# Performance work log

Hardware: AMD Instinct MI355X
Metric: run time of the kernel (lower is better)

## Reference

```python
import jax, jax.numpy as jnp
import numpy as np

B, LQ, LK = 8, 256, 256
Q_SIZE = K_SIZE = H = D_V = 256
MASK_VALUE = -1000000.0


def setup_inputs() -> dict:
    key = jax.random.key(0)
    kq, kk, kv, kl, kwq, kwk, kwv = jax.random.split(key, 7)
    # Linear weights, torch nn.Linear stores (out, in); init ~ U(-1/sqrt(in), 1/sqrt(in))
    def lin(k, out_f, in_f):
        bound = 1.0 / np.sqrt(in_f)
        return jax.random.uniform(k, (out_f, in_f), jnp.float32, -bound, bound)
    return {
        "queries": jax.random.normal(kq, (B, LQ, Q_SIZE), jnp.float32),
        "keyes": jax.random.normal(kk, (B, LK, K_SIZE), jnp.float32),
        "values": jax.random.normal(kv, (B, LK, D_V), jnp.float32),
        "valid_lens": jax.random.randint(kl, (B,), 1, LK + 1),
        "W_q": lin(kwq, H, Q_SIZE),
        "W_k": lin(kwk, H, K_SIZE),
        "W_v": lin(kwv, 1, H),
    }


def reference(queries, keyes, values, valid_lens, W_q, W_k, W_v):
    # Projections (nn.Linear without bias): x @ W.T
    q = jnp.einsum("bqd,hd->bqh", queries, W_q)            # (B, Lq, H)
    k = jnp.einsum("bkd,hd->bkh", keyes, W_k)              # (B, Lk, H)
    # Broadcast-add + tanh: (B, Lq, Lk, H)
    features = jnp.tanh(q[:, :, None, :] + k[:, None, :, :])
    # W_v reduction H -> 1, squeeze: scores (B, Lq, Lk)
    scores = jnp.einsum("bqkh,h->bqk", features, W_v[0])
    # sequence_mask over the last (key) axis with value -1e6
    lk = scores.shape[-1]
    mask = jnp.arange(lk)[None, None, :] < valid_lens[:, None, None]  # (B,1,Lk)
    scores = jnp.where(mask, scores, MASK_VALUE)
    # NOTE: this repo's masked_softmax normalizes over dim=1 (the query axis),
    # faithfully reproduced here.
    attention_weights = jax.nn.softmax(scores, axis=1)
    # dropout is identity in eval / p=0.0
    return jnp.einsum("bqk,bkd->bqd", attention_weights, values)
```

## Files before the change

kernel.cpp:

```cpp
#include <hip/hip_runtime.h>

typedef float vf4 __attribute__((ext_vector_type(4)));

#define LOG2E 1.4426950408889634f
#define TWO_LOG2E 2.8853900817779268f

__device__ __forceinline__ float fexp2(float x) { return __builtin_amdgcn_exp2f(x); }
__device__ __forceinline__ float frcp(float x) { return __builtin_amdgcn_rcpf(x); }

__global__ __launch_bounds__(256) void proj_kernel(
    const float* __restrict__ queries, const float* __restrict__ keyes,
    const float* __restrict__ Wq, const float* __restrict__ Wk,
    float* __restrict__ QpH, float* __restrict__ KpH,
    float* __restrict__ Rsum) {
  __shared__ alignas(16) float At[16 * 68];
  __shared__ alignas(16) float Bt[16 * 68];
  const int t = threadIdx.x;
  if (blockIdx.x == 0 && blockIdx.y == 0 && blockIdx.z == 0) {
    *(vf4*)&Rsum[t * 8] = (vf4){0.f, 0.f, 0.f, 0.f};
    *(vf4*)&Rsum[t * 8 + 4] = (vf4){0.f, 0.f, 0.f, 0.f};
  }
  const int m0 = blockIdx.x * 64;
  const int n0 = blockIdx.y * 64;
  const int k0 = blockIdx.z * 128;
  const bool isQ = (m0 < 2048);
  const float* X = isQ ? queries : keyes;
  const float* W = isQ ? Wq : Wk;
  float* C = (isQ ? QpH : KpH) + blockIdx.z * 524288;
  const int mb = isQ ? m0 : (m0 - 2048);

  const int lm = t >> 2;
  const int lq = t & 3;
  const int mm4 = (t & 15) * 4;
  const int nn4 = (t >> 4) * 4;

  float acc[4][4] = {};
  for (int kc = k0; kc < k0 + 128; kc += 16) {
    __syncthreads();
    vf4 xa = *(const vf4*)&X[(mb + lm) * 256 + kc + lq * 4];
    vf4 wb = *(const vf4*)&W[(n0 + lm) * 256 + kc + lq * 4];
#pragma unroll
    for (int c = 0; c < 4; ++c) {
      At[(lq * 4 + c) * 68 + lm] = xa[c];
      Bt[(lq * 4 + c) * 68 + lm] = wb[c];
    }
    __syncthreads();
#pragma unroll
    for (int kk = 0; kk < 16; ++kk) {
      vf4 a4 = *(const vf4*)&At[kk * 68 + mm4];
      vf4 b4 = *(const vf4*)&Bt[kk * 68 + nn4];
#pragma unroll
      for (int i = 0; i < 4; ++i)
#pragma unroll
        for (int j = 0; j < 4; ++j) acc[i][j] += a4[i] * b4[j];
    }
  }
#pragma unroll
  for (int i = 0; i < 4; ++i) {
    vf4 o = {fexp2(acc[i][0] * TWO_LOG2E), fexp2(acc[i][1] * TWO_LOG2E),
             fexp2(acc[i][2] * TWO_LOG2E), fexp2(acc[i][3] * TWO_LOG2E)};
    *(vf4*)&C[(mb + mm4 + i) * 256 + n0 + nn4] = o;
  }
}

__global__ __launch_bounds__(256) void scores_exp_kernel(
    const float* __restrict__ QpH, const float* __restrict__ KpH,
    const float* __restrict__ Wv, const int* __restrict__ valid_lens,
    float* __restrict__ E, float* __restrict__ Rsum) {
  __shared__ alignas(16) float Qs[32 * 32];
  __shared__ alignas(16) float Ks[32 * 32];
  const int t = threadIdx.x;
  const int i0 = blockIdx.x * 32;
  const int j0 = blockIdx.y * 32;
  const int b = blockIdx.z;
  const int ti = t & 15;
  const int tj = t >> 4;

  float Swv;
  {
    vf4 w4 = *(const vf4*)&Wv[(t & 63) * 4];
    float sw = w4[0] + w4[1] + w4[2] + w4[3];
#pragma unroll
    for (int off = 1; off < 64; off <<= 1) sw += __shfl_xor(sw, off, 64);
    Swv = sw;
  }

  const int srow = t >> 3;
  const int scg = t & 7;
  const int swcol = ((scg ^ (srow & 7)) << 2);
  const int qxor = ti & 7;
  const int kxor = tj & 7;

  float acc[2][2] = {};
  for (int hc = 0; hc < 8; ++hc) {
    __syncthreads();
    const int qoff = (((b << 8) + i0 + srow) << 8) + hc * 32 + scg * 4;
    const int koff = (((b << 8) + j0 + srow) << 8) + hc * 32 + scg * 4;
    vf4 qv = *(const vf4*)&QpH[qoff];
    vf4 qv2 = *(const vf4*)&QpH[524288 + qoff];
    vf4 kv = *(const vf4*)&KpH[koff];
    vf4 kv2 = *(const vf4*)&KpH[524288 + koff];
    *(vf4*)&Qs[srow * 32 + swcol] = qv * qv2;
    *(vf4*)&Ks[srow * 32 + swcol] = kv * kv2;
    __syncthreads();
#pragma unroll
    for (int hh = 0; hh < 8; ++hh) {
      vf4 q0 = *(const vf4*)&Qs[ti * 32 + ((hh ^ qxor) << 2)];
      vf4 q1 = *(const vf4*)&Qs[(ti + 16) * 32 + ((hh ^ qxor) << 2)];
      vf4 k0 = *(const vf4*)&Ks[tj * 32 + ((hh ^ kxor) << 2)];
      vf4 k1 = *(const vf4*)&Ks[(tj + 16) * 32 + ((hh ^ kxor) << 2)];
      const int hb = hc * 32 + hh * 4;
      const float w0 = Wv[hb + 0];
      const float w1 = Wv[hb + 1];
      const float w2 = Wv[hb + 2];
      const float w3 = Wv[hb + 3];
      auto term = [&](const vf4& q, const vf4& k, float& a) {
        float A0 = __builtin_fmaf(q[0], k[0], 1.0f);
        float A1 = __builtin_fmaf(q[1], k[1], 1.0f);
        float A2 = __builtin_fmaf(q[2], k[2], 1.0f);
        float A3 = __builtin_fmaf(q[3], k[3], 1.0f);
        float d01 = A0 * A1;
        float d23 = A2 * A3;
        float n01 = __builtin_fmaf(w0, A1, w1 * A0);
        float n23 = __builtin_fmaf(w2, A3, w3 * A2);
        float num = __builtin_fmaf(n01, d23, n23 * d01);
        a = __builtin_fmaf(num, frcp(d01 * d23), a);
      };
      term(q0, k0, acc[0][0]);
      term(q0, k1, acc[0][1]);
      term(q1, k0, acc[1][0]);
      term(q1, k1, acc[1][1]);
    }
  }

  const int len = valid_lens[b];
#pragma unroll
  for (int c = 0; c < 2; ++c) {
    const int j = j0 + tj + 16 * c;
    const bool masked = (j >= len);
    float ev[2];
#pragma unroll
    for (int r = 0; r < 2; ++r) {
      const int i = i0 + ti + 16 * r;
      const float score = Swv - 2.0f * acc[r][c];
      ev[r] = masked ? 1.0f : fexp2(score * LOG2E);
      E[(((b << 8) + j) << 8) + i] = ev[r];
    }
    float s = ev[0] + ev[1];
#pragma unroll
    for (int off = 1; off < 16; off <<= 1) s += __shfl_xor(s, off, 64);
    if (ti == 0) atomicAdd(&Rsum[(b << 8) + j], s);
  }
}

__global__ __launch_bounds__(256) void out_kernel(
    const float* __restrict__ E, const float* __restrict__ Rsum,
    const float* __restrict__ V, float* __restrict__ out) {
  __shared__ alignas(16) float As[32 * 36];
  __shared__ alignas(16) float Bs[32 * 68];
  const int t = threadIdx.x;
  const int i0 = blockIdx.x * 32;
  const int d0 = blockIdx.y * 64;
  const int b = blockIdx.z;
  const int ti = t & 15;
  const int td = t >> 4;
  const int sr = t >> 3;
  const int sc4 = (t & 7) * 4;

  float acc[2][4] = {};
  for (int jc = 0; jc < 8; ++jc) {
    const int jb = jc * 32;
    __syncthreads();
    const float rj = frcp(Rsum[(b << 8) + jb + sr]);
    {
      vf4 a = *(const vf4*)&E[(((b << 8) + jb + sr) << 8) + i0 + sc4];
      *(vf4*)&As[sr * 36 + sc4] = a * rj;
    }
#pragma unroll
    for (int s = 0; s < 2; ++s) {
      const int col = sc4 + s * 32;
      *(vf4*)&Bs[sr * 68 + col] =
          *(const vf4*)&V[(((b << 8) + jb + sr) << 8) + d0 + col];
    }
    __syncthreads();
#pragma unroll
    for (int j = 0; j < 32; ++j) {
      const float a0 = As[j * 36 + ti];
      const float a1 = As[j * 36 + ti + 16];
      vf4 b4 = *(const vf4*)&Bs[j * 68 + td * 4];
#pragma unroll
      for (int c = 0; c < 4; ++c) {
        acc[0][c] += a0 * b4[c];
        acc[1][c] += a1 * b4[c];
      }
    }
  }
#pragma unroll
  for (int r = 0; r < 2; ++r) {
    vf4 o = {acc[r][0], acc[r][1], acc[r][2], acc[r][3]};
    *(vf4*)&out[(((b << 8) + i0 + ti + 16 * r) << 8) + d0 + td * 4] = o;
  }
}

extern "C" void kernel_launch(void* const* d_in, const int* in_sizes, int n_in,
                              void* d_out, int out_size, void* d_ws, size_t ws_size,
                              hipStream_t stream) {
  const float* queries = (const float*)d_in[0];
  const float* keyes = (const float*)d_in[1];
  const float* values = (const float*)d_in[2];
  const int* valid_lens = (const int*)d_in[3];
  const float* Wq = (const float*)d_in[4];
  const float* Wk = (const float*)d_in[5];
  const float* Wv = (const float*)d_in[6];
  float* out = (float*)d_out;

  float* QpH = (float*)d_ws;
  float* KpH = QpH + 2 * 524288;
  float* E = KpH + 2 * 524288;
  float* Rsum = E + 524288;

  proj_kernel<<<dim3(64, 4, 2), 256, 0, stream>>>(queries, keyes, Wq, Wk,
                                                  QpH, KpH, Rsum);
  scores_exp_kernel<<<dim3(8, 8, 8), 256, 0, stream>>>(QpH, KpH, Wv,
                                                       valid_lens, E, Rsum);
  out_kernel<<<dim3(8, 4, 8), 256, 0, stream>>>(E, Rsum, values, out);
}
```

Measured before the change: 107.5 us.

## Restructure projection GEMM with full W tile in LDS and double-buffered X

The projection kernel now uses 128 threads with an 8x4 register tile per thread. The whole 128x64 weight slice is loaded into shared memory once, and the activation tiles are double-buffered with register prefetch, so one barrier per k-step replaces two. The goal is more FMA work per LDS load and less synchronisation, paid for with more shared memory per block and fewer threads per block. Separately, the output kernel reads its two A values as one vf2 load by remapping rows so each thread owns two adjacent rows.

Result: slower. 114.5 us (+6.6%).

```diff
diff --git a/kernel.cpp b/kernel.cpp
--- a/kernel.cpp
+++ b/kernel.cpp
@@ -1,6 +1,7 @@
 #include <hip/hip_runtime.h>
 
 typedef float vf4 __attribute__((ext_vector_type(4)));
+typedef float vf2 __attribute__((ext_vector_type(2)));
 
 #define LOG2E 1.4426950408889634f
 #define TWO_LOG2E 2.8853900817779268f
@@ -8,17 +9,18 @@
 __device__ __forceinline__ float fexp2(float x) { return __builtin_amdgcn_exp2f(x); }
 __device__ __forceinline__ float frcp(float x) { return __builtin_amdgcn_rcpf(x); }
 
-__global__ __launch_bounds__(256) void proj_kernel(
+__global__ __launch_bounds__(128) void proj_kernel(
     const float* __restrict__ queries, const float* __restrict__ keyes,
     const float* __restrict__ Wq, const float* __restrict__ Wk,
     float* __restrict__ QpH, float* __restrict__ KpH,
     float* __restrict__ Rsum) {
-  __shared__ alignas(16) float At[16 * 68];
-  __shared__ alignas(16) float Bt[16 * 68];
+  __shared__ alignas(16) float Bs[128 * 68];
+  __shared__ alignas(16) float At[2][16 * 68];
   const int t = threadIdx.x;
   if (blockIdx.x == 0 && blockIdx.y == 0 && blockIdx.z == 0) {
-    *(vf4*)&Rsum[t * 8] = (vf4){0.f, 0.f, 0.f, 0.f};
-    *(vf4*)&Rsum[t * 8 + 4] = (vf4){0.f, 0.f, 0.f, 0.f};
+#pragma unroll
+    for (int c = 0; c < 4; ++c)
+      *(vf4*)&Rsum[t * 16 + c * 4] = (vf4){0.f, 0.f, 0.f, 0.f};
   }
   const int m0 = blockIdx.x * 64;
   const int n0 = blockIdx.y * 64;
@@ -29,37 +31,74 @@
   float* C = (isQ ? QpH : KpH) + blockIdx.z * 524288;
   const int mb = isQ ? m0 : (m0 - 2048);
 
-  const int lm = t >> 2;
-  const int lq = t & 3;
-  const int mm4 = (t & 15) * 4;
-  const int nn4 = (t >> 4) * 4;
-
-  float acc[4][4] = {};
-  for (int kc = k0; kc < k0 + 128; kc += 16) {
-    __syncthreads();
-    vf4 xa = *(const vf4*)&X[(mb + lm) * 256 + kc + lq * 4];
-    vf4 wb = *(const vf4*)&W[(n0 + lm) * 256 + kc + lq * 4];
-#pragma unroll
-    for (int c = 0; c < 4; ++c) {
-      At[(lq * 4 + c) * 68 + lm] = xa[c];
-      Bt[(lq * 4 + c) * 68 + lm] = wb[c];
-    }
-    __syncthreads();
+  {
+    const int wn = t & 63;
+    const int wh = t >> 6;
+    const float* wsrc = &W[(n0 + wn) * 256 + k0 + wh * 64];
+#pragma unroll
+    for (int c4 = 0; c4 < 64; c4 += 4) {
+      vf4 wv = *(const vf4*)&wsrc[c4];
+#pragma unroll
+      for (int e = 0; e < 4; ++e) Bs[(wh * 64 + c4 + e) * 68 + wn] = wv[e];
+    }
+  }
+
+  const int lm = t >> 1;
+  const int lq = t & 1;
+  vf4 ra0, ra1;
+  {
+    const float* src = &X[(mb + lm) * 256 + k0 + lq * 8];
+    ra0 = *(const vf4*)src;
+    ra1 = *(const vf4*)(src + 4);
+#pragma unroll
+    for (int c = 0; c < 4; ++c) At[0][(lq * 8 + c) * 68 + lm] = ra0[c];
+#pragma unroll
+    for (int c = 0; c < 4; ++c) At[0][(lq * 8 + 4 + c) * 68 + lm] = ra1[c];
+    src = &X[(mb + lm) * 256 + k0 + 16 + lq * 8];
+    ra0 = *(const vf4*)src;
+    ra1 = *(const vf4*)(src + 4);
+  }
+  __syncthreads();
+
+  const int tm8 = (t & 7) * 8;
+  const int tn4 = (t >> 3) * 4;
+
+  float acc[8][4] = {};
+#pragma unroll
+  for (int s = 0; s < 8; ++s) {
+    if (s < 7) {
+#pragma unroll
+      for (int c = 0; c < 4; ++c) At[(s + 1) & 1][(lq * 8 + c) * 68 + lm] = ra0[c];
+#pragma unroll
+      for (int c = 0; c < 4; ++c) At[(s + 1) & 1][(lq * 8 + 4 + c) * 68 + lm] = ra1[c];
+    }
+    if (s < 6) {
+      const float* src = &X[(mb + lm) * 256 + k0 + (s + 2) * 16 + lq * 8];
+      ra0 = *(const vf4*)src;
+      ra1 = *(const vf4*)(src + 4);
+    }
+    const float* ab = At[s & 1];
+    const float* bb = &Bs[s * 16 * 68];
 #pragma unroll
     for (int kk = 0; kk < 16; ++kk) {
-      vf4 a4 = *(const vf4*)&At[kk * 68 + mm4];
-      vf4 b4 = *(const vf4*)&Bt[kk * 68 + nn4];
+      vf4 a0 = *(const vf4*)&ab[kk * 68 + tm8];
+      vf4 a1 = *(const vf4*)&ab[kk * 68 + tm8 + 4];
+      vf4 b4 = *(const vf4*)&bb[kk * 68 + tn4];
 #pragma unroll
       for (int i = 0; i < 4; ++i)
 #pragma unroll
-        for (int j = 0; j < 4; ++j) acc[i][j] += a4[i] * b4[j];
-    }
-  }
-#pragma unroll
-  for (int i = 0; i < 4; ++i) {
+        for (int j = 0; j < 4; ++j) {
+          acc[i][j] += a0[i] * b4[j];
+          acc[i + 4][j] += a1[i] * b4[j];
+        }
+    }
+    if (s < 7) __syncthreads();
+  }
+#pragma unroll
+  for (int i = 0; i < 8; ++i) {
     vf4 o = {fexp2(acc[i][0] * TWO_LOG2E), fexp2(acc[i][1] * TWO_LOG2E),
              fexp2(acc[i][2] * TWO_LOG2E), fexp2(acc[i][3] * TWO_LOG2E)};
-    *(vf4*)&C[(mb + mm4 + i) * 256 + n0 + nn4] = o;
+    *(vf4*)&C[(mb + tm8 + i) * 256 + n0 + tn4] = o;
   }
 }
 
@@ -185,20 +224,19 @@
     __syncthreads();
 #pragma unroll
     for (int j = 0; j < 32; ++j) {
-      const float a0 = As[j * 36 + ti];
-      const float a1 = As[j * 36 + ti + 16];
+      vf2 a = *(const vf2*)&As[j * 36 + 2 * ti];
       vf4 b4 = *(const vf4*)&Bs[j * 68 + td * 4];
 #pragma unroll
       for (int c = 0; c < 4; ++c) {
-        acc[0][c] += a0 * b4[c];
-        acc[1][c] += a1 * b4[c];
+        acc[0][c] += a[0] * b4[c];
+        acc[1][c] += a[1] * b4[c];
       }
     }
   }
 #pragma unroll
   for (int r = 0; r < 2; ++r) {
     vf4 o = {acc[r][0], acc[r][1], acc[r][2], acc[r][3]};
-    *(vf4*)&out[(((b << 8) + i0 + ti + 16 * r) << 8) + d0 + td * 4] = o;
+    *(vf4*)&out[(((b << 8) + i0 + 2 * ti + r) << 8) + d0 + td * 4] = o;
   }
 }
 
@@ -219,7 +257,7 @@
   float* E = KpH + 2 * 524288;
   float* Rsum = E + 524288;
 
-  proj_kernel<<<dim3(64, 4, 2), 256, 0, stream>>>(queries, keyes, Wq, Wk,
+  proj_kernel<<<dim3(64, 4, 2), 128, 0, stream>>>(queries, keyes, Wq, Wk,
                                                   QpH, KpH, Rsum);
   scores_exp_kernel<<<dim3(8, 8, 8), 256, 0, stream>>>(QpH, KpH, Wv,
                                                        valid_lens, E, Rsum);
```
